# Optimization experiments

Measured on AMD Instinct MI355X. Metric: run time of the kernel, lower is better.

The kernel has to match this reference:

```python
import jax, jax.numpy as jnp
import numpy as np

V, E, H, B = 32000, 1024, 2048, 512


def setup_inputs() -> dict:
    key = jax.random.key(0)
    ks = jax.random.split(key, 9)
    s = 0.02
    emb_table = jax.random.normal(ks[0], (V, E), jnp.float32) * s
    emb_table = emb_table.at[0].set(0.0)  # padding_idx=0
    W_ih = jax.random.normal(ks[1], (3 * H, E), jnp.float32) * s  # gates [r,z,n]
    W_hh = jax.random.normal(ks[2], (3 * H, H), jnp.float32) * s
    b_ih = jax.random.normal(ks[3], (3 * H,), jnp.float32) * s
    b_hh = jax.random.normal(ks[4], (3 * H,), jnp.float32) * s
    fc_W = jax.random.normal(ks[5], (V, H), jnp.float32) * s
    fc_b = jax.random.normal(ks[6], (V,), jnp.float32) * s
    input_step = jax.random.randint(ks[7], (B,), 0, V, jnp.int64)
    hidden = jax.random.normal(ks[8], (1, B, H), jnp.float32)
    return {"input_step": input_step, "hidden": hidden, "emb_table": emb_table,
            "W_ih": W_ih, "W_hh": W_hh, "b_ih": b_ih, "b_hh": b_hh,
            "fc_W": fc_W, "fc_b": fc_b}


def reference(input_step, hidden, emb_table, W_ih, W_hh, b_ih, b_hh, fc_W, fc_b):
    # Embedding lookup (seq_len=1, so the unsqueeze/squeeze cancel)
    x = emb_table[input_step]                       # [B, E]
    h = hidden[0]                                   # [B, H]
    # Single GRU step, PyTorch gate order [r, z, n]
    gi = x @ W_ih.T + b_ih                          # [B, 3H]
    gh = h @ W_hh.T + b_hh                          # [B, 3H]
    gi_r, gi_z, gi_n = jnp.split(gi, 3, axis=-1)
    gh_r, gh_z, gh_n = jnp.split(gh, 3, axis=-1)
    r = jax.nn.sigmoid(gi_r + gh_r)
    z = jax.nn.sigmoid(gi_z + gh_z)
    n = jnp.tanh(gi_n + r * gh_n)
    h_new = (1.0 - z) * n + z * h                   # [B, H]
    logits = h_new @ fc_W.T + fc_b                  # [B, V]
    return logits, h_new[None]                      # hidden back as [1, B, H]
```

## Files before the change

kernel.cpp:

```cpp
#include <hip/hip_runtime.h>
#include <hip/hip_bf16.h>

typedef __attribute__((ext_vector_type(8))) short short8;
typedef __attribute__((ext_vector_type(4))) short short4v;
typedef __attribute__((ext_vector_type(4))) float f32x4;

__device__ __forceinline__ short f2bf(float f) {
  union { __hip_bfloat16 h; short s; } u;
  u.h = __float2bfloat16(f);
  return u.s;
}

__device__ __forceinline__ void gll16(const void* g, void* l) {
  __builtin_amdgcn_global_load_lds(
      (const __attribute__((address_space(1))) void*)g,
      (__attribute__((address_space(3))) void*)l, 16, 0, 0);
}

#define SCHED_FENCE() __builtin_amdgcn_sched_barrier(0)

template<int BF>
__device__ __forceinline__ void gemm_dma(
    const short* __restrict__ A,
    const float* __restrict__ W,
    const float* __restrict__ bias,
    float* __restrict__ C,
    int K, int N, int n0, char* smem)
{
  constexpr int WOPS   = BF / 4;
  constexpr int WBYTES = BF * 16 * 128;
  constexpr int ABYTES = 512 * 64;
  constexpr int BUNDLE = 4 + WOPS;
  constexpr int WAIT   = 2 * BUNDLE;

  const int t   = threadIdx.x;
  const int w   = t >> 6;
  const int l   = t & 63;
  const int l16 = l & 15;
  const int lq  = l >> 4;

  f32x4 acc[4][BF];
  #pragma unroll
  for (int i = 0; i < 4; ++i)
    #pragma unroll
    for (int j = 0; j < BF; ++j) {
      f32x4 z = {0.f, 0.f, 0.f, 0.f};
      acc[i][j] = z;
    }

  const int arow0  = w * 64 + (l >> 2);
  const int aslot  = (l & 3) ^ ((l >> 3) & 3);
  const int wslot  = (l & 7) ^ (l >> 3);
  const int wrow0  = n0 + w * 8 + (l >> 3);

  auto issueBundle = [&](int bi) {
    const int buf = bi % 3;
    const int kb  = bi << 5;
    char* ab = smem + 3 * WBYTES + buf * ABYTES;
    char* wb = smem + buf * WBYTES;
    #pragma unroll
    for (int j = 0; j < 4; ++j)
      gll16(A + (size_t)(arow0 + j * 16) * K + kb + aslot * 8,
            ab + w * 4096 + j * 1024);
    #pragma unroll
    for (int o = 0; o < WOPS; ++o)
      gll16(W + (size_t)(wrow0 + o * 64) * K + kb + wslot * 4,
            wb + o * 8192 + w * 1024);
  };

  auto consume = [&](int bi) {
    const int buf = bi % 3;
    const char* ab = smem + 3 * WBYTES + buf * ABYTES;
    const char* wb = smem + buf * WBYTES;
    short8 a[4];
    const int asw = (lq ^ ((l16 >> 1) & 3)) * 16;
    #pragma unroll
    for (int mf = 0; mf < 4; ++mf)
      a[mf] = *(const short8*)(ab + (w * 64 + mf * 16 + l16) * 64 + asw);
    const int x = l16 & 7;
    #pragma unroll
    for (int nf = 0; nf < BF; ++nf) {
      const int row = nf * 16 + l16;
      f32x4 u = *(const f32x4*)(wb + row * 128 + ((2 * lq) ^ x) * 16);
      f32x4 v = *(const f32x4*)(wb + row * 128 + ((2 * lq + 1) ^ x) * 16);
      short8 b;
      #pragma unroll
      for (int i = 0; i < 4; ++i) { b[i] = f2bf(u[i]); b[i + 4] = f2bf(v[i]); }
      #pragma unroll
      for (int mf = 0; mf < 4; ++mf)
        acc[mf][nf] = __builtin_amdgcn_mfma_f32_16x16x32_bf16(a[mf], b, acc[mf][nf], 0, 0, 0);
    }
  };

  issueBundle(0); issueBundle(1); issueBundle(2);

  const int nt = K >> 5;
  for (int b = 0; b < nt - 3; ++b) {
    asm volatile("s_waitcnt vmcnt(%0)" :: "n"(WAIT) : "memory");
    SCHED_FENCE();
    __builtin_amdgcn_s_barrier();
    SCHED_FENCE();
    consume(b);
    asm volatile("s_waitcnt lgkmcnt(0)" ::: "memory");
    SCHED_FENCE();
    __builtin_amdgcn_s_barrier();
    SCHED_FENCE();
    issueBundle(b + 3);
  }
  asm volatile("s_waitcnt vmcnt(0)" ::: "memory");
  SCHED_FENCE();
  __builtin_amdgcn_s_barrier();
  SCHED_FENCE();
  consume(nt - 3); consume(nt - 2); consume(nt - 1);
  __syncthreads();

  constexpr int BN  = BF * 16;
  constexpr int EPS = BN + 4;
  constexpr int CPR = BN / 4;
  float bvv[BF];
  #pragma unroll
  for (int nf = 0; nf < BF; ++nf) bvv[nf] = bias[n0 + nf * 16 + l16];

  float* ep = (float*)(smem) + w * 16 * EPS;
  const int erow = l / CPR;
  const int ecol = (l % CPR) * 4;
  #pragma unroll
  for (int mf = 0; mf < 4; ++mf) {
    #pragma unroll
    for (int nf = 0; nf < BF; ++nf)
      #pragma unroll
      for (int r = 0; r < 4; ++r)
        ep[(lq * 4 + r) * EPS + nf * 16 + l16] = acc[mf][nf][r] + bvv[nf];
    #pragma unroll
    for (int i = 0; i < BF; ++i) {
      const int row = i * (16 / BF) + erow;
      f32x4 vv = *(const f32x4*)&ep[row * EPS + ecol];
      *(f32x4*)&C[(size_t)(w * 64 + mf * 16 + row) * N + n0 + ecol] = vv;
    }
  }
}

__global__ __launch_bounds__(512, 2) void gru_gemms_kernel(
    const short* __restrict__ xbf, const short* __restrict__ hbf,
    const float* __restrict__ W_ih, const float* __restrict__ W_hh,
    const float* __restrict__ b_ih, const float* __restrict__ b_hh,
    float* __restrict__ gi, float* __restrict__ gh)
{
  __shared__ char smem[3 * (4 * 16 * 128) + 3 * 32768];
  const bool second = blockIdx.x >= 96;
  const int nb = second ? (int)blockIdx.x - 96 : (int)blockIdx.x;
  gemm_dma<4>(second ? hbf : xbf,
              second ? W_hh : W_ih,
              second ? b_hh : b_ih,
              second ? gh : gi,
              second ? 2048 : 1024,
              6144, nb * 64, smem);
}

__global__ __launch_bounds__(512, 2) void logits_kernel(
    const short* __restrict__ hnbf, const float* __restrict__ fc_W,
    const float* __restrict__ fc_b, float* __restrict__ out)
{
  __shared__ char smem[3 * (8 * 16 * 128) + 3 * 32768];
  gemm_dma<8>(hnbf, fc_W, fc_b, out, 2048, 32000, (int)blockIdx.x * 128, smem);
}

__global__ void prep_kernel(const int* __restrict__ idx,
                            const float* __restrict__ hid,
                            const float* __restrict__ emb,
                            short* __restrict__ xbf, short* __restrict__ hbf)
{
  int i = blockIdx.x * blockDim.x + threadIdx.x;
  const int NX = 512 * 1024 / 4;
  const int NH = 512 * 2048 / 4;
  if (i < NX) {
    int b = i >> 8;
    int c = (i & 255) << 2;
    int row = idx[b];
    f32x4 v = *(const f32x4*)(emb + (size_t)row * 1024 + c);
    short4v o;
    #pragma unroll
    for (int j = 0; j < 4; ++j) o[j] = f2bf(v[j]);
    *(short4v*)(xbf + (size_t)b * 1024 + c) = o;
  } else if (i < NX + NH) {
    int j2 = i - NX;
    f32x4 v = *(const f32x4*)(hid + (size_t)j2 * 4);
    short4v o;
    #pragma unroll
    for (int j = 0; j < 4; ++j) o[j] = f2bf(v[j]);
    *(short4v*)(hbf + (size_t)j2 * 4) = o;
  }
}

__global__ void gates_kernel(const float* __restrict__ gi,
                             const float* __restrict__ gh,
                             const float* __restrict__ hid,
                             float* __restrict__ hnew,
                             short* __restrict__ hnbf)
{
  int i = blockIdx.x * blockDim.x + threadIdx.x;
  int b = i >> 9;
  int c = (i & 511) << 2;
  size_t gbase = (size_t)b * 6144 + c;
  f32x4 gir = *(const f32x4*)(gi + gbase);
  f32x4 giz = *(const f32x4*)(gi + gbase + 2048);
  f32x4 gin = *(const f32x4*)(gi + gbase + 4096);
  f32x4 ghr = *(const f32x4*)(gh + gbase);
  f32x4 ghz = *(const f32x4*)(gh + gbase + 2048);
  f32x4 ghn = *(const f32x4*)(gh + gbase + 4096);
  f32x4 hv  = *(const f32x4*)(hid + (size_t)b * 2048 + c);
  f32x4 hn;
  short4v hb;
  #pragma unroll
  for (int j = 0; j < 4; ++j) {
    float r = 1.f / (1.f + __expf(-(gir[j] + ghr[j])));
    float z = 1.f / (1.f + __expf(-(giz[j] + ghz[j])));
    float n = tanhf(gin[j] + r * ghn[j]);
    float o = (1.f - z) * n + z * hv[j];
    hn[j] = o;
    hb[j] = f2bf(o);
  }
  *(f32x4*)(hnew + (size_t)b * 2048 + c) = hn;
  *(short4v*)(hnbf + (size_t)b * 2048 + c) = hb;
}

extern "C" void kernel_launch(void* const* d_in, const int* in_sizes, int n_in,
                              void* d_out, int out_size, void* d_ws, size_t ws_size,
                              hipStream_t stream)
{
  const int*   idx   = (const int*)d_in[0];
  const float* hid   = (const float*)d_in[1];
  const float* emb   = (const float*)d_in[2];
  const float* W_ih  = (const float*)d_in[3];
  const float* W_hh  = (const float*)d_in[4];
  const float* b_ih  = (const float*)d_in[5];
  const float* b_hh  = (const float*)d_in[6];
  const float* fc_W  = (const float*)d_in[7];
  const float* fc_b  = (const float*)d_in[8];
  float* out = (float*)d_out;

  char* ws = (char*)d_ws;
  short* xbf  = (short*)(ws);
  short* hbf  = (short*)(ws + 1048576);
  short* hnbf = (short*)(ws + 3145728);
  float* gi   = (float*)(ws + 5242880);
  float* gh   = (float*)(ws + 17825792);

  prep_kernel<<<1536, 256, 0, stream>>>(idx, hid, emb, xbf, hbf);
  gru_gemms_kernel<<<192, 512, 0, stream>>>(xbf, hbf, W_ih, W_hh, b_ih, b_hh, gi, gh);
  gates_kernel<<<1024, 256, 0, stream>>>(gi, gh, hid, out + (size_t)512 * 32000, hnbf);
  logits_kernel<<<250, 512, 0, stream>>>(hnbf, fc_W, fc_b, out);
}
```

Baseline: 196.3 us.

## Load A fragments directly to registers, drop A LDS staging and one barrier

The A (activation) tiles are now loaded straight from global memory into registers, double-buffered one k-step ahead, rather than DMA'd into LDS and read back. Only the weight tiles still go through LDS, now in a 4-slot ring with 3 in flight, so the second per-iteration barrier and lgkmcnt wait are gone. This shrinks shared memory and removes the A LDS round trip. In exchange, A loads become uncoalesced per-lane 16-byte global reads that share the vmcnt counter with the weight DMAs, and more registers are used. The epilogue loop bound is also recomputed so it stays correct for both tile widths.

New measurement: 237.2 us. 1.21x slower.

```diff
diff --git a/kernel.cpp b/kernel.cpp
--- a/kernel.cpp
+++ b/kernel.cpp
@@ -27,11 +27,8 @@
     float* __restrict__ C,
     int K, int N, int n0, char* smem)
 {
-  constexpr int WOPS   = BF / 4;
-  constexpr int WBYTES = BF * 16 * 128;
-  constexpr int ABYTES = 512 * 64;
-  constexpr int BUNDLE = 4 + WOPS;
-  constexpr int WAIT   = 2 * BUNDLE;
+  constexpr int WOPS = BF / 4;
+  constexpr int WBUF = BF * 16 * 128;
 
   const int t   = threadIdx.x;
   const int w   = t >> 6;
@@ -48,35 +45,26 @@
       acc[i][j] = z;
     }
 
-  const int arow0  = w * 64 + (l >> 2);
-  const int aslot  = (l & 3) ^ ((l >> 3) & 3);
-  const int wslot  = (l & 7) ^ (l >> 3);
-  const int wrow0  = n0 + w * 8 + (l >> 3);
-
-  auto issueBundle = [&](int bi) {
-    const int buf = bi % 3;
-    const int kb  = bi << 5;
-    char* ab = smem + 3 * WBYTES + buf * ABYTES;
-    char* wb = smem + buf * WBYTES;
-    #pragma unroll
-    for (int j = 0; j < 4; ++j)
-      gll16(A + (size_t)(arow0 + j * 16) * K + kb + aslot * 8,
-            ab + w * 4096 + j * 1024);
+  const int wslot = (l & 7) ^ (l >> 3);
+  const int wrow0 = n0 + w * 8 + (l >> 3);
+  const short* ap = A + (size_t)(w * 64 + l16) * K + lq * 8;
+
+  auto issueW = [&](int bi) {
+    char* wb = smem + (bi & 3) * WBUF;
+    const int kb = bi << 5;
     #pragma unroll
     for (int o = 0; o < WOPS; ++o)
       gll16(W + (size_t)(wrow0 + o * 64) * K + kb + wslot * 4,
             wb + o * 8192 + w * 1024);
   };
-
-  auto consume = [&](int bi) {
-    const int buf = bi % 3;
-    const char* ab = smem + 3 * WBYTES + buf * ABYTES;
-    const char* wb = smem + buf * WBYTES;
-    short8 a[4];
-    const int asw = (lq ^ ((l16 >> 1) & 3)) * 16;
+  auto issueA = [&](int bi, short8 (&a)[4]) {
+    const int kb = bi << 5;
     #pragma unroll
     for (int mf = 0; mf < 4; ++mf)
-      a[mf] = *(const short8*)(ab + (w * 64 + mf * 16 + l16) * 64 + asw);
+      a[mf] = *(const short8*)(ap + (size_t)mf * 16 * K + kb);
+  };
+  auto consume = [&](int bi, short8 (&a)[4]) {
+    const char* wb = smem + (bi & 3) * WBUF;
     const int x = l16 & 7;
     #pragma unroll
     for (int nf = 0; nf < BF; ++nf) {
@@ -92,26 +80,27 @@
     }
   };
 
-  issueBundle(0); issueBundle(1); issueBundle(2);
-
   const int nt = K >> 5;
-  for (int b = 0; b < nt - 3; ++b) {
-    asm volatile("s_waitcnt vmcnt(%0)" :: "n"(WAIT) : "memory");
+  short8 aA[4], aB[4];
+
+  issueA(0, aA);
+  issueW(0); issueW(1); issueW(2);
+
+  auto step = [&](int b, short8 (&aCur)[4], short8 (&aNext)[4]) {
+    if (b + 2 < nt) { asm volatile("s_waitcnt vmcnt(%0)" :: "n"(WOPS) : "memory"); }
+    else            { asm volatile("s_waitcnt vmcnt(0)" ::: "memory"); }
     SCHED_FENCE();
     __builtin_amdgcn_s_barrier();
     SCHED_FENCE();
-    consume(b);
-    asm volatile("s_waitcnt lgkmcnt(0)" ::: "memory");
-    SCHED_FENCE();
-    __builtin_amdgcn_s_barrier();
-    SCHED_FENCE();
-    issueBundle(b + 3);
-  }
-  asm volatile("s_waitcnt vmcnt(0)" ::: "memory");
-  SCHED_FENCE();
-  __builtin_amdgcn_s_barrier();
-  SCHED_FENCE();
-  consume(nt - 3); consume(nt - 2); consume(nt - 1);
+    if (b + 1 < nt) issueA(b + 1, aNext);
+    consume(b, aCur);
+    if (b + 3 < nt) issueW(b + 3);
+  };
+
+  for (int b = 0; b < nt; b += 2) {
+    step(b,     aA, aB);
+    step(b + 1, aB, aA);
+  }
   __syncthreads();
 
   constexpr int BN  = BF * 16;
@@ -132,8 +121,8 @@
       for (int r = 0; r < 4; ++r)
         ep[(lq * 4 + r) * EPS + nf * 16 + l16] = acc[mf][nf][r] + bvv[nf];
     #pragma unroll
-    for (int i = 0; i < BF; ++i) {
-      const int row = i * (16 / BF) + erow;
+    for (int i = 0; i < 16 / (64 / CPR); ++i) {
+      const int row = i * (64 / CPR) + erow;
       f32x4 vv = *(const f32x4*)&ep[row * EPS + ecol];
       *(f32x4*)&C[(size_t)(w * 64 + mf * 16 + row) * N + n0 + ecol] = vv;
     }
@@ -146,7 +135,7 @@
     const float* __restrict__ b_ih, const float* __restrict__ b_hh,
     float* __restrict__ gi, float* __restrict__ gh)
 {
-  __shared__ char smem[3 * (4 * 16 * 128) + 3 * 32768];
+  __shared__ __align__(16) char smem[34816];
   const bool second = blockIdx.x >= 96;
   const int nb = second ? (int)blockIdx.x - 96 : (int)blockIdx.x;
   gemm_dma<4>(second ? hbf : xbf,
@@ -161,7 +150,7 @@
     const short* __restrict__ hnbf, const float* __restrict__ fc_W,
     const float* __restrict__ fc_b, float* __restrict__ out)
 {
-  __shared__ char smem[3 * (8 * 16 * 128) + 3 * 32768];
+  __shared__ __align__(16) char smem[67584];
   gemm_dma<8>(hnbf, fc_W, fc_b, out, 2048, 32000, (int)blockIdx.x * 128, smem);
 }
 
```
